# Performance work log

Hardware: AMD Instinct MI355X
Metric: run time of the kernel (lower is better)

## Reference

```python
import jax, jax.numpy as jnp
import numpy as np

B, N, F_IN, F_OUT = 4, 4096, 64, 64
ALPHA = 0.2  # LeakyReLU negative slope
NEG_INF = -9e15


def setup_inputs() -> dict:
    key = jax.random.key(0)
    k1, k2, k3, k4 = jax.random.split(key, 4)
    h = jax.random.normal(k1, (B, N, F_IN), dtype=jnp.float32)
    adj = jax.random.randint(k2, (B, N, N), 0, 2, dtype=jnp.int32)
    # xavier_uniform-like init (gain 1.414)
    lim_w = 1.414 * np.sqrt(6.0 / (F_IN + F_OUT))
    W = jax.random.uniform(k3, (F_IN, F_OUT), dtype=jnp.float32, minval=-lim_w, maxval=lim_w)
    lim_a = 1.414 * np.sqrt(6.0 / (2 * F_OUT + 1))
    a = jax.random.uniform(k4, (2 * F_OUT, 1), dtype=jnp.float32, minval=-lim_a, maxval=lim_a)
    return {"h": h, "adj": adj, "W": W, "a": a}


def reference(h, adj, W, a):
    # Wh: [B, N, F_out]
    Wh = jnp.matmul(h, W)
    a1 = a[:F_OUT, 0]   # [F_out]
    a2 = a[F_OUT:, 0]   # [F_out]
    # e[b,i,j] = LeakyReLU(Wh[b,i].a1 + Wh[b,j].a2)  (decomposed, avoids O(N^2*2F) concat)
    ei = jnp.einsum('bnf,f->bn', Wh, a1)  # source term
    ej = jnp.einsum('bnf,f->bn', Wh, a2)  # target term
    e = ei[:, :, None] + ej[:, None, :]   # [B, N, N]
    e = jnp.where(e > 0, e, ALPHA * e)    # LeakyReLU
    att = jnp.where(adj > 0, e, NEG_INF)
    att = jax.nn.softmax(att, axis=-1)
    h_prime = jnp.matmul(att, Wh)         # [B, N, F_out]
    return jax.nn.elu(h_prime)
```

## Files before the change

### kernel.cpp

```cpp
#include <hip/hip_runtime.h>
#include <stdint.h>

#define N_NODES 4096
#define F_DIM   64
#define LRELU_ALPHA 0.2f

typedef _Float16 f16;
typedef __attribute__((ext_vector_type(8))) _Float16 half8;
typedef __attribute__((ext_vector_type(4))) float f32x4;

__global__ __launch_bounds__(256) void gat_prep(
    const float* __restrict__ h, const float* __restrict__ W,
    const float* __restrict__ a, float* __restrict__ ei,
    float* __restrict__ ej, f16* __restrict__ wh16,
    float* __restrict__ blockmax)
{
  __shared__ float sh_h[4][F_DIM];
  __shared__ f16 tile[F_DIM][16];
  __shared__ float wmax[4];
  const int t = threadIdx.x, w = t >> 6, lane = t & 63;
  const int n0 = blockIdx.x * 16;
  const int b  = n0 >> 12;
  const int nl0 = n0 & (N_NODES - 1);

  float wcol[F_DIM];
#pragma unroll
  for (int k = 0; k < F_DIM; ++k) wcol[k] = W[k * F_DIM + lane];
  const float a1 = a[lane], a2 = a[F_DIM + lane];

  float runmax = -3e38f;
  for (int r = 0; r < 4; ++r) {
    const int loc = w * 4 + r;
    const int n = n0 + loc;
    const float hv = h[(size_t)n * F_DIM + lane];
    sh_h[w][lane] = hv;
    float wh = 0.f;
#pragma unroll
    for (int k = 0; k < F_DIM; k += 4) {
      const float4 hb = *(const float4*)(&sh_h[w][k]);
      wh = fmaf(hb.x, wcol[k + 0], wh);
      wh = fmaf(hb.y, wcol[k + 1], wh);
      wh = fmaf(hb.z, wcol[k + 2], wh);
      wh = fmaf(hb.w, wcol[k + 3], wh);
    }
    float s1 = wh * a1, s2 = wh * a2;
#pragma unroll
    for (int off = 32; off; off >>= 1) {
      s1 += __shfl_xor(s1, off);
      s2 += __shfl_xor(s2, off);
    }
    if (lane == 0) { ei[n] = s1; ej[n] = s2; }
    runmax = fmaxf(runmax, s2);
    tile[lane][loc] = (f16)wh;
  }
  if (lane == 0) wmax[w] = runmax;
  __syncthreads();

  {
    const int f = t >> 2, part = t & 3;
    *(uint2*)(wh16 + ((size_t)(b * F_DIM + f)) * N_NODES + nl0 + part * 4) =
        *(const uint2*)(&tile[f][part * 4]);
  }
  if (t == 0)
    blockmax[blockIdx.x] =
        fmaxf(fmaxf(wmax[0], wmax[1]), fmaxf(wmax[2], wmax[3]));
}

__global__ __launch_bounds__(512, 6) void gat_attn(
    const int* __restrict__ adj, const float* __restrict__ ei,
    const float* __restrict__ ej, const f16* __restrict__ wh16,
    const float* __restrict__ blockmax, float* __restrict__ out)
{
  __shared__ float num_lds[8][16][F_DIM];
  __shared__ float den_lds[8][16];

  const int t = threadIdx.x, w = t >> 6, lane = t & 63;
  const int quad = lane >> 4, m = lane & 15;
  const int b  = blockIdx.x >> 8;
  const int i0 = (blockIdx.x & 255) * 16;
  const int i  = i0 + m;
  const int rowg = b * N_NODES + i;

  float maxej;
  {
    const float4 v = *(const float4*)(blockmax + b * 256 + lane * 4);
    maxej = fmaxf(fmaxf(v.x, v.y), fmaxf(v.z, v.w));
#pragma unroll
    for (int off = 32; off; off >>= 1)
      maxej = fmaxf(maxej, __shfl_xor(maxej, off));
  }

  const float ei_s = ei[rowg];
  float bnd = ei_s + maxej;
  bnd = fmaxf(bnd, LRELU_ALPHA * bnd);

  const float* ejb     = ej + b * N_NODES;
  const int*   adj_row = adj + (size_t)rowg * N_NODES;
  const f16*   whb     = wh16 + ((size_t)(b * F_DIM + m)) * N_NODES;

  f32x4 acc[4] = {{0.f,0.f,0.f,0.f},{0.f,0.f,0.f,0.f},
                  {0.f,0.f,0.f,0.f},{0.f,0.f,0.f,0.f}};
  float den = 0.f;
  const int jbase = w * (N_NODES / 8);

  for (int jc = 0; jc < 16; ++jc) {
    const int jk = jbase + jc * 32 + quad * 8;

    float ejA[8];
    *(float4*)(&ejA[0]) = *(const float4*)(ejb + jk);
    *(float4*)(&ejA[4]) = *(const float4*)(ejb + jk + 4);
    int adA[8];
    *(int4*)(&adA[0]) = *(const int4*)(adj_row + jk);
    *(int4*)(&adA[4]) = *(const int4*)(adj_row + jk + 4);

    half8 bf[4];
#pragma unroll
    for (int fc = 0; fc < 4; ++fc)
      bf[fc] = *(const half8*)(whb + (size_t)(fc * 16) * N_NODES + jk);

    half8 pa;
#pragma unroll
    for (int x = 0; x < 8; ++x) {
      float e = ei_s + ejA[x];
      e = fmaxf(e, LRELU_ALPHA * e);
      const float p = (adA[x] > 0) ? __expf(e - bnd) : 0.f;
      pa[x] = (f16)p;
      den += (float)pa[x];
    }

#pragma unroll
    for (int fc = 0; fc < 4; ++fc)
      acc[fc] = __builtin_amdgcn_mfma_f32_16x16x32_f16(pa, bf[fc], acc[fc], 0, 0, 0);
  }

  den += __shfl_xor(den, 16);
  den += __shfl_xor(den, 32);
  if (lane < 16) den_lds[w][lane] = den;

#pragma unroll
  for (int fc = 0; fc < 4; ++fc)
#pragma unroll
    for (int rg = 0; rg < 4; ++rg)
      num_lds[w][quad * 4 + rg][fc * 16 + m] = acc[fc][rg];
  __syncthreads();

#pragma unroll
  for (int k = 0; k < 2; ++k) {
    const int idx = k * 512 + t;
    const int il = idx >> 6, f = idx & 63;
    float num = 0.f, d = 0.f;
#pragma unroll
    for (int ww = 0; ww < 8; ++ww) {
      num += num_lds[ww][il][f];
      d   += den_lds[ww][il];
    }
    float v = (d > 0.f) ? (num / d) : 0.f;
    v = (v > 0.f) ? v : expm1f(v);
    out[((size_t)(b * N_NODES + i0 + il)) * F_DIM + f] = v;
  }
}

extern "C" void kernel_launch(void* const* d_in, const int* in_sizes, int n_in,
                              void* d_out, int out_size, void* d_ws, size_t ws_size,
                              hipStream_t stream) {
  const float* h   = (const float*)d_in[0];
  const int*   adj = (const int*)d_in[1];
  const float* W   = (const float*)d_in[2];
  const float* a   = (const float*)d_in[3];
  float* out = (float*)d_out;

  char* ws = (char*)d_ws;
  float* ei       = (float*)ws;
  float* ej       = (float*)(ws + 65536);
  float* blockmax = (float*)(ws + 131072);
  f16*   wh16     = (f16*)(ws + 135168);

  hipLaunchKernelGGL(gat_prep, dim3(1024), dim3(256), 0, stream,
                     h, W, a, ei, ej, wh16, blockmax);
  hipLaunchKernelGGL(gat_attn, dim3(1024), dim3(512), 0, stream,
                     adj, ei, ej, wh16, blockmax, out);
}
```

Measured before the change: 416.9 us.

## Pack adjacency into bitmask in a separate streaming kernel before attention

Adds a pre-pass kernel that reads the int32 adjacency matrix with coalesced vector loads and writes one bit per edge. The attention kernel then reads 32x less mask data per row, replacing its scattered per-lane int4 adjacency loads with a few uint4 bitmask loads. The full adjacency is still read once, plus an extra launch and an 8MB bitmask write and read.

```diff
diff --git a/kernel.cpp b/kernel.cpp
--- a/kernel.cpp
+++ b/kernel.cpp
@@ -8,6 +8,25 @@
 typedef _Float16 f16;
 typedef __attribute__((ext_vector_type(8))) _Float16 half8;
 typedef __attribute__((ext_vector_type(4))) float f32x4;
+
+__global__ __launch_bounds__(256) void gat_pack(
+    const int* __restrict__ adj, uint32_t* __restrict__ bits)
+{
+  const int idx = blockIdx.x * 256 + threadIdx.x;
+  const int r   = idx >> 7;
+  const int jw  = idx & 127;
+  const int* p = adj + (size_t)r * N_NODES + jw * 32;
+  uint32_t mask = 0;
+#pragma unroll
+  for (int k = 0; k < 8; ++k) {
+    const int4 v = *(const int4*)(p + k * 4);
+    mask |= (v.x > 0 ? 1u : 0u) << (k * 4 + 0);
+    mask |= (v.y > 0 ? 1u : 0u) << (k * 4 + 1);
+    mask |= (v.z > 0 ? 1u : 0u) << (k * 4 + 2);
+    mask |= (v.w > 0 ? 1u : 0u) << (k * 4 + 3);
+  }
+  bits[idx] = mask;
+}
 
 __global__ __launch_bounds__(256) void gat_prep(
     const float* __restrict__ h, const float* __restrict__ W,
@@ -67,7 +86,7 @@
 }
 
 __global__ __launch_bounds__(512, 6) void gat_attn(
-    const int* __restrict__ adj, const float* __restrict__ ei,
+    const uint32_t* __restrict__ bits, const float* __restrict__ ei,
     const float* __restrict__ ej, const f16* __restrict__ wh16,
     const float* __restrict__ blockmax, float* __restrict__ out)
 {
@@ -95,7 +114,7 @@
   bnd = fmaxf(bnd, LRELU_ALPHA * bnd);
 
   const float* ejb     = ej + b * N_NODES;
-  const int*   adj_row = adj + (size_t)rowg * N_NODES;
+  const uint32_t* bitrow = bits + (size_t)rowg * 128 + w * 16;
   const f16*   whb     = wh16 + ((size_t)(b * F_DIM + m)) * N_NODES;
 
   f32x4 acc[4] = {{0.f,0.f,0.f,0.f},{0.f,0.f,0.f,0.f},
@@ -103,34 +122,40 @@
   float den = 0.f;
   const int jbase = w * (N_NODES / 8);
 
-  for (int jc = 0; jc < 16; ++jc) {
-    const int jk = jbase + jc * 32 + quad * 8;
-
-    float ejA[8];
-    *(float4*)(&ejA[0]) = *(const float4*)(ejb + jk);
-    *(float4*)(&ejA[4]) = *(const float4*)(ejb + jk + 4);
-    int adA[8];
-    *(int4*)(&adA[0]) = *(const int4*)(adj_row + jk);
-    *(int4*)(&adA[4]) = *(const int4*)(adj_row + jk + 4);
-
-    half8 bf[4];
-#pragma unroll
-    for (int fc = 0; fc < 4; ++fc)
-      bf[fc] = *(const half8*)(whb + (size_t)(fc * 16) * N_NODES + jk);
-
-    half8 pa;
-#pragma unroll
-    for (int x = 0; x < 8; ++x) {
-      float e = ei_s + ejA[x];
-      e = fmaxf(e, LRELU_ALPHA * e);
-      const float p = (adA[x] > 0) ? __expf(e - bnd) : 0.f;
-      pa[x] = (f16)p;
-      den += (float)pa[x];
-    }
-
-#pragma unroll
-    for (int fc = 0; fc < 4; ++fc)
-      acc[fc] = __builtin_amdgcn_mfma_f32_16x16x32_f16(pa, bf[fc], acc[fc], 0, 0, 0);
+  for (int jo = 0; jo < 4; ++jo) {
+    const uint4 dq = *(const uint4*)(bitrow + jo * 4);
+    const uint32_t dws[4] = {dq.x, dq.y, dq.z, dq.w};
+
+#pragma unroll
+    for (int ji = 0; ji < 4; ++ji) {
+      const int jc = jo * 4 + ji;
+      const int jk = jbase + jc * 32 + quad * 8;
+      const uint32_t dw = dws[ji];
+
+      float ejA[8];
+      *(float4*)(&ejA[0]) = *(const float4*)(ejb + jk);
+      *(float4*)(&ejA[4]) = *(const float4*)(ejb + jk + 4);
+
+      half8 bf[4];
+#pragma unroll
+      for (int fc = 0; fc < 4; ++fc)
+        bf[fc] = *(const half8*)(whb + (size_t)(fc * 16) * N_NODES + jk);
+
+      half8 pa;
+#pragma unroll
+      for (int x = 0; x < 8; ++x) {
+        float e = ei_s + ejA[x];
+        e = fmaxf(e, LRELU_ALPHA * e);
+        const float p =
+            ((dw >> (quad * 8 + x)) & 1u) ? __expf(e - bnd) : 0.f;
+        pa[x] = (f16)p;
+        den += (float)pa[x];
+      }
+
+#pragma unroll
+      for (int fc = 0; fc < 4; ++fc)
+        acc[fc] = __builtin_amdgcn_mfma_f32_16x16x32_f16(pa, bf[fc], acc[fc], 0, 0, 0);
+    }
   }
 
   den += __shfl_xor(den, 16);
@@ -170,13 +195,15 @@
   float* out = (float*)d_out;
 
   char* ws = (char*)d_ws;
-  float* ei       = (float*)ws;
-  float* ej       = (float*)(ws + 65536);
-  float* blockmax = (float*)(ws + 131072);
-  f16*   wh16     = (f16*)(ws + 135168);
-
+  float*    ei       = (float*)ws;
+  float*    ej       = (float*)(ws + 65536);
+  float*    blockmax = (float*)(ws + 131072);
+  f16*      wh16     = (f16*)(ws + 135168);
+  uint32_t* bits     = (uint32_t*)(ws + 2232320);
+
+  hipLaunchKernelGGL(gat_pack, dim3(8192), dim3(256), 0, stream, adj, bits);
   hipLaunchKernelGGL(gat_prep, dim3(1024), dim3(256), 0, stream,
                      h, W, a, ei, ej, wh16, blockmax);
   hipLaunchKernelGGL(gat_attn, dim3(1024), dim3(512), 0, stream,
-                     adj, ei, ej, wh16, blockmax, out);
-}
+                     bits, ei, ej, wh16, blockmax, out);
+}
```

New measurement: 445.8 us. 6.9% more time.
